# Kernel optimization log

Hardware: AMD Instinct MI355X
Metric: run time of the kernel (lower is better)

## Reference

```python
import jax, jax.numpy as jnp
import numpy as np

GRID = (128, 128, 16)
VSIZE = 0.5  # voxel_size, pc_range = 0
B, V, N, K, C = 2, 100000, 8192, 8, 64
EPS = 1e-5
OFFSETS = [(dx, dy, dz) for dx in (-1, 0, 1) for dy in (-1, 0, 1) for dz in (-1, 0, 1)]


def setup_inputs() -> dict:
    key = jax.random.key(0)
    ks = jax.random.split(key, 8)
    world = jnp.array([GRID[0] * VSIZE, GRID[1] * VSIZE, GRID[2] * VSIZE], jnp.float32)
    keypoints = jax.random.uniform(ks[0], (B, N, K, 3), jnp.float32) * world
    query_feature = jax.random.normal(ks[1], (B, N, C), jnp.float32)
    voxel_feature = jax.random.normal(ks[2], (B, V, C), jnp.float32)
    # unique voxel coords per batch (hash-map / sparse-tensor semantics)
    cells = GRID[0] * GRID[1] * GRID[2]
    perm = jax.vmap(lambda k: jax.random.permutation(k, cells)[:V])(jax.random.split(ks[3], B))
    x = perm // (GRID[1] * GRID[2])
    rem = perm % (GRID[1] * GRID[2])
    voxel_coords = jnp.stack([x, rem // GRID[2], rem % GRID[2]], -1).astype(jnp.int32)
    W1 = jax.random.normal(ks[4], (27, C, C), jnp.float32) * 0.05
    W2 = jax.random.normal(ks[5], (27, C, C), jnp.float32) * 0.05
    proj_W = jax.random.normal(ks[6], (C, C), jnp.float32) / np.sqrt(C).astype(np.float32)
    proj_b = jnp.zeros((C,), jnp.float32)
    return dict(keypoints=keypoints, query_feature=query_feature,
                voxel_feature=voxel_feature, voxel_coords=voxel_coords,
                W1=W1, bn1_gamma=jnp.ones((C,), jnp.float32), bn1_beta=jnp.zeros((C,), jnp.float32),
                W2=W2, bn2_gamma=jnp.ones((C,), jnp.float32), bn2_beta=jnp.zeros((C,), jnp.float32),
                proj_W=proj_W, proj_b=proj_b)


def _subm_conv(feats, grid, cb, cxyz, W):
    # feats: (M, C); grid: (B, X, Y, Z) int32 flat row index or -1; W: (27, Cin, Cout)
    out = jnp.zeros((feats.shape[0], W.shape[-1]), feats.dtype)
    for k, (dx, dy, dz) in enumerate(OFFSETS):
        nx, ny, nz = cxyz[:, 0] + dx, cxyz[:, 1] + dy, cxyz[:, 2] + dz
        valid = (nx >= 0) & (nx < GRID[0]) & (ny >= 0) & (ny < GRID[1]) & (nz >= 0) & (nz < GRID[2])
        nidx = grid[cb, jnp.clip(nx, 0, GRID[0] - 1), jnp.clip(ny, 0, GRID[1] - 1), jnp.clip(nz, 0, GRID[2] - 1)]
        nidx = jnp.where(valid, nidx, -1)
        nf = jnp.where((nidx >= 0)[:, None], feats[jnp.maximum(nidx, 0)], jnp.zeros((), feats.dtype))
        out = out + nf @ W[k]
    return out


def _bn_relu(x, gamma, beta):
    # BatchNorm1d in training mode: batch stats (biased var), then ReLU
    mu = x.mean(0)
    var = jnp.var(x, axis=0)
    return jax.nn.relu((x - mu) * jax.lax.rsqrt(var + EPS) * gamma + beta)


def reference(keypoints, query_feature, voxel_feature, voxel_coords,
              W1, bn1_gamma, bn1_beta, W2, bn2_gamma, bn2_beta, proj_W, proj_b):
    coords = voxel_coords.reshape(-1, 3).astype(jnp.int32)
    cb = jnp.repeat(jnp.arange(B, dtype=jnp.int32), V)
    # dense grid hash: cell -> flat voxel row, -1 if empty (replaces Python dict)
    grid = jnp.full((B,) + GRID, -1, jnp.int32)
    grid = grid.at[cb, coords[:, 0], coords[:, 1], coords[:, 2]].set(jnp.arange(B * V, dtype=jnp.int32))
    feats = voxel_feature.reshape(-1, C)
    feats = _bn_relu(_subm_conv(feats, grid, cb, coords, W1), bn1_gamma, bn1_beta)
    feats = _bn_relu(_subm_conv(feats, grid, cb, coords, W2), bn2_gamma, bn2_beta)
    # quantize keypoints (pc_range = 0, trunc == floor since coords >= 0)
    q = (keypoints / VSIZE).astype(jnp.int32)
    q = jnp.clip(q, 0, jnp.array(GRID, jnp.int32) - 1)  # (B, N, K, 3)
    bidx = jnp.arange(B, dtype=jnp.int32)[:, None, None]
    idx = grid[bidx, q[..., 0], q[..., 1], q[..., 2]]   # (B, N, K); -1 -> fallback row 0
    sampled = feats[jnp.maximum(idx, 0)]                 # (B, N, K, C)
    fused = (sampled.mean(2) + query_feature) @ proj_W.T + proj_b
    voxel_indices = jnp.concatenate(
        [jnp.broadcast_to(bidx[..., None], (B, N, K, 1)), q], axis=-1).reshape(-1, 4)
    return fused, voxel_indices
```

## Files before the change

kernel.cpp:

```cpp
#include <hip/hip_runtime.h>
#include <hip/hip_bf16.h>
#include <math.h>

#define GX 128
#define GY 128
#define GZ 16
#define CELLS (GX*GY*GZ)
#define NCELLT (NB*CELLS)
#define NB 2
#define NV 100000
#define NM (NB*NV)
#define NN 8192
#define NK 8
#define NC 64
#define EPSV 1e-5f
#define TM 256
#define NTILE 98
#define NBLK (8*NTILE)
#define KPH 7

typedef __attribute__((ext_vector_type(8))) short short8;
typedef __attribute__((ext_vector_type(4))) float floatx4;

__device__ __forceinline__ float bf2f(unsigned short u) {
    unsigned int x = ((unsigned int)u) << 16;
    return __builtin_bit_cast(float, x);
}
__device__ __forceinline__ unsigned short f2bf(float f) {
    unsigned int u = __builtin_bit_cast(unsigned int, f);
    return (unsigned short)((u + 0x7fffu + ((u >> 16) & 1u)) >> 16);
}

__global__ void k_init(int* __restrict__ grid, float* __restrict__ stats,
                       unsigned short* __restrict__ featA) {
    int i = blockIdx.x * 256 + threadIdx.x;
    if (i < NCELLT) grid[i] = -1;
    else if (i < NCELLT + 512) stats[i - NCELLT] = 0.f;
    else if (i < NCELLT + 512 + 64) featA[(size_t)NM * 64 + (i - NCELLT - 512)] = 0;
}

__global__ void k_scatter(const int* __restrict__ coords, int* __restrict__ grid) {
    int gid = blockIdx.x * 256 + threadIdx.x;
    if (gid >= NM) return;
    int b = (gid >= NV) ? 1 : 0;
    int x = coords[gid * 3 + 0];
    int y = coords[gid * 3 + 1];
    int z = coords[gid * 3 + 2];
    grid[((b * GX + x) * GY + y) * GZ + z] = gid;
}

__global__ void k_count(const int* __restrict__ grid, int* __restrict__ bcnt) {
    __shared__ int wt[4];
    int t = threadIdx.x;
    int occ = (grid[blockIdx.x * 256 + t] >= 0) ? 1 : 0;
    int w = t >> 6;
    unsigned long long m = __ballot(occ);
    if ((t & 63) == 0) wt[w] = __popcll(m);
    __syncthreads();
    if (t == 0) bcnt[blockIdx.x] = wt[0] + wt[1] + wt[2] + wt[3];
}

__global__ void k_scan2048(const int* __restrict__ bcnt, int* __restrict__ boff) {
    __shared__ int s[256];
    int t = threadIdx.x;
    int v[8], sum = 0;
    #pragma unroll
    for (int j = 0; j < 8; ++j) {
        int x = bcnt[t * 8 + j];
        v[j] = sum;
        sum += x;
    }
    s[t] = sum;
    __syncthreads();
    for (int off = 1; off < 256; off <<= 1) {
        int x = (t >= off) ? s[t - off] : 0;
        __syncthreads();
        s[t] += x;
        __syncthreads();
    }
    int excl = s[t] - sum;
    #pragma unroll
    for (int j = 0; j < 8; ++j) boff[t * 8 + j] = excl + v[j];
}

__global__ void k_assign(const int* __restrict__ gold, const int* __restrict__ boff,
                         int* __restrict__ gnew, int* __restrict__ perm,
                         int* __restrict__ scell) {
    __shared__ int wt[4];
    int t = threadIdx.x;
    int cell = blockIdx.x * 256 + t;
    int old = gold[cell];
    int occ = (old >= 0) ? 1 : 0;
    int w = t >> 6, lane = t & 63;
    unsigned long long m = __ballot(occ);
    int lp = __popcll(m & ((1ULL << lane) - 1ULL));
    if (lane == 63) wt[w] = lp + occ;
    __syncthreads();
    int wbase = 0;
    #pragma unroll
    for (int j = 0; j < 4; ++j) if (j < w) wbase += wt[j];
    int nid = boff[blockIdx.x] + wbase + lp;
    if (occ) {
        gnew[cell] = nid;
        perm[nid] = old;
        scell[nid] = cell;
    } else {
        gnew[cell] = -1;
    }
}

__global__ void k_fb(const int* __restrict__ vcoords, const int* __restrict__ gnew,
                     int* __restrict__ fbp) {
    if (threadIdx.x == 0 && blockIdx.x == 0) {
        int cell = (vcoords[0] * GY + vcoords[1]) * GZ + vcoords[2];
        fbp[0] = gnew[cell];
    }
}

__global__ void k_wprep(const float* __restrict__ W1, const float* __restrict__ W2,
                        unsigned short* __restrict__ Wt1, unsigned short* __restrict__ Wt2) {
    int e = blockIdx.x * 256 + threadIdx.x;
    if (e >= 28 * 512) return;
    int lane = e & 63;
    int fr = (e >> 6) & 7;
    int k = e >> 9;
    int ct = fr >> 1, ks = fr & 1;
    int quad = lane >> 4, n16 = lane & 15;
    int co = ct * 16 + n16;
    #pragma unroll
    for (int j = 0; j < 8; ++j) {
        int ci = ks * 32 + quad * 8 + j;
        unsigned short w1 = 0, w2 = 0;
        if (k < 27) {
            w1 = f2bf(W1[(k << 12) + ci * 64 + co]);
            w2 = f2bf(W2[(k << 12) + ci * 64 + co]);
        }
        Wt1[(size_t)e * 8 + j] = w1;
        Wt2[(size_t)e * 8 + j] = w2;
    }
}

__global__ void k_tobf16s(const float* __restrict__ in, const int* __restrict__ perm,
                          unsigned short* __restrict__ out) {
    int i = blockIdx.x * 256 + threadIdx.x;
    if (i >= NM * 8) return;
    int mrow = i >> 3, part = i & 7;
    int src = perm[mrow];
    const float4* s = (const float4*)(in + (size_t)src * 64 + part * 8);
    float4 a = s[0], b = s[1];
    ushort4 lo, hi;
    lo.x = f2bf(a.x); lo.y = f2bf(a.y); lo.z = f2bf(a.z); lo.w = f2bf(a.w);
    hi.x = f2bf(b.x); hi.y = f2bf(b.y); hi.z = f2bf(b.z); hi.w = f2bf(b.w);
    ushort4* d = (ushort4*)(out + (size_t)mrow * 64 + part * 8);
    d[0] = lo; d[1] = hi;
}

__global__ __launch_bounds__(256, 2) void k_conv(
    const unsigned short* __restrict__ feats, const int* __restrict__ scell,
    const int* __restrict__ grid, const unsigned short* __restrict__ Wt,
    unsigned short* __restrict__ out, float* __restrict__ gsum, float* __restrict__ gsq)
{
    __shared__ unsigned short s_b[KPH * 4096];
    __shared__ int s_nidx[KPH * TM];
    __shared__ int s_c[TM];

    int tid = threadIdx.x;
    int bid = blockIdx.x;
    int tile = (bid & 7) * NTILE + (bid >> 3);
    int m0 = tile * TM;

    {
        int m = m0 + tid;
        s_c[tid] = (m < NM) ? scell[m] : -1;
    }

    int w = tid >> 6, lane = tid & 63;
    int quad = lane >> 4, n16 = lane & 15;
    const unsigned short* fq = feats + quad * 8;

    short8 afr[2][8];

    auto issueA = [&](int kk, short8* af) {
        #pragma unroll
        for (int rt = 0; rt < 4; ++rt) {
            int ni = s_nidx[kk * TM + w * 64 + rt * 16 + n16];
            ni = (ni < 0) ? NM : ni;
            const unsigned short* r0 = fq + (size_t)ni * 64;
            af[rt * 2 + 0] = *(const short8*)(r0);
            af[rt * 2 + 1] = *(const short8*)(r0 + 32);
        }
    };

    floatx4 acc[4][4];
    #pragma unroll
    for (int rt = 0; rt < 4; ++rt)
        #pragma unroll
        for (int ct = 0; ct < 4; ++ct)
            acc[rt][ct] = (floatx4){0.f, 0.f, 0.f, 0.f};

    const uint4* wt4 = (const uint4*)Wt;

    for (int ph = 0; ph < 4; ++ph) {
        int k0 = ph * KPH;
        __syncthreads();
        #pragma unroll
        for (int i = 0; i < KPH * 2; ++i)
            ((uint4*)s_b)[i * 256 + tid] = wt4[(size_t)k0 * 512 + i * 256 + tid];
        #pragma unroll
        for (int j = 0; j < KPH; ++j) {
            int e = j * 256 + tid;
            int kk = e >> 8;
            int r = e & 255;
            int k = k0 + kk;
            int ni = -1;
            if (k < 27) {
                int dx = k / 9 - 1, dy = (k / 3) % 3 - 1, dz = k % 3 - 1;
                int cell = s_c[r];
                if (cell >= 0) {
                    int x = (cell >> 11) & 127, y = (cell >> 4) & 127, z = cell & 15;
                    int nx = x + dx, ny = y + dy, nz = z + dz;
                    if (nx >= 0 && nx < GX && ny >= 0 && ny < GY && nz >= 0 && nz < GZ)
                        ni = grid[cell + dx * (GY * GZ) + dy * GZ + dz];
                }
            }
            s_nidx[kk * TM + r] = ni;
        }
        __syncthreads();

        issueA(0, afr[0]);
        __builtin_amdgcn_sched_barrier(0);

        #pragma unroll
        for (int kk = 0; kk < KPH; ++kk) {
            if (kk + 1 < KPH) issueA(kk + 1, afr[(kk + 1) & 1]);
            __builtin_amdgcn_sched_barrier(0);

            const unsigned short* bb = s_b + kk * 4096;
            short8 bfr[8];
            #pragma unroll
            for (int fr = 0; fr < 8; ++fr)
                bfr[fr] = *(const short8*)(bb + fr * 512 + lane * 8);

            const short8* ac = afr[kk & 1];
            #pragma unroll
            for (int ks = 0; ks < 2; ++ks)
                #pragma unroll
                for (int rt = 0; rt < 4; ++rt)
                    #pragma unroll
                    for (int ct = 0; ct < 4; ++ct)
                        acc[rt][ct] = __builtin_amdgcn_mfma_f32_16x16x32_bf16(
                            ac[rt * 2 + ks], bfr[ct * 2 + ks], acc[rt][ct], 0, 0, 0);
            __builtin_amdgcn_sched_barrier(0);
        }
    }

    #pragma unroll
    for (int rt = 0; rt < 4; ++rt) {
        int rbase = m0 + w * 64 + rt * 16 + quad * 4;
        #pragma unroll
        for (int rg = 0; rg < 4; ++rg) {
            int m = rbase + rg;
            if (m < NM) {
                #pragma unroll
                for (int ct = 0; ct < 4; ++ct)
                    out[(size_t)m * 64 + ct * 16 + n16] = f2bf(acc[rt][ct][rg]);
            }
        }
    }

    float ps[4], pq[4];
    #pragma unroll
    for (int ct = 0; ct < 4; ++ct) { ps[ct] = 0.f; pq[ct] = 0.f; }
    #pragma unroll
    for (int rt = 0; rt < 4; ++rt)
        #pragma unroll
        for (int ct = 0; ct < 4; ++ct)
            #pragma unroll
            for (int rg = 0; rg < 4; ++rg) {
                float v = acc[rt][ct][rg];
                ps[ct] += v;
                pq[ct] += v * v;
            }
    #pragma unroll
    for (int ct = 0; ct < 4; ++ct) {
        ps[ct] += __shfl_xor(ps[ct], 16);
        ps[ct] += __shfl_xor(ps[ct], 32);
        pq[ct] += __shfl_xor(pq[ct], 16);
        pq[ct] += __shfl_xor(pq[ct], 32);
    }
    __syncthreads();
    float* red = (float*)s_nidx;
    if (lane < 16) {
        #pragma unroll
        for (int ct = 0; ct < 4; ++ct) {
            red[w * 64 + ct * 16 + n16]       = ps[ct];
            red[256 + w * 64 + ct * 16 + n16] = pq[ct];
        }
    }
    __syncthreads();
    if (tid < 64) {
        float ts = 0.f, tq = 0.f;
        #pragma unroll
        for (int ww = 0; ww < 4; ++ww) {
            ts += red[ww * 64 + tid];
            tq += red[256 + ww * 64 + tid];
        }
        atomicAdd(gsum + tid, ts);
        atomicAdd(gsq + tid, tq);
    }
}

__global__ void k_bncoef(const float* __restrict__ gsum, const float* __restrict__ gsq,
                         const float* __restrict__ gamma, const float* __restrict__ beta,
                         float* __restrict__ coef) {
    int c = threadIdx.x;
    if (c >= 64) return;
    float mu = gsum[c] / (float)NM;
    float var = gsq[c] / (float)NM - mu * mu;
    float scale = gamma[c] / sqrtf(var + EPSV);
    coef[c] = scale;
    coef[64 + c] = beta[c] - mu * scale;
}

__global__ void k_bnapply(const unsigned short* __restrict__ in, const float* __restrict__ coef,
                          unsigned short* __restrict__ out) {
    int i = blockIdx.x * 256 + threadIdx.x;
    if (i >= NM * 8) return;
    int c8 = (i & 7) * 8;
    uint4 v = ((const uint4*)in)[i];
    unsigned int vv[4] = {v.x, v.y, v.z, v.w};
    unsigned int oo[4];
    #pragma unroll
    for (int j = 0; j < 4; ++j) {
        int c = c8 + j * 2;
        float lo = bf2f((unsigned short)(vv[j] & 0xffffu));
        float hi = bf2f((unsigned short)(vv[j] >> 16));
        lo = fmaxf(lo * coef[c]     + coef[64 + c],     0.f);
        hi = fmaxf(hi * coef[c + 1] + coef[64 + c + 1], 0.f);
        oo[j] = (unsigned int)f2bf(lo) | ((unsigned int)f2bf(hi) << 16);
    }
    uint4 o = {oo[0], oo[1], oo[2], oo[3]};
    ((uint4*)out)[i] = o;
}

__global__ __launch_bounds__(256) void k_sample(
    const float* __restrict__ kp, const float* __restrict__ query,
    const unsigned short* __restrict__ conv2, const float* __restrict__ coef2,
    const int* __restrict__ grid, const int* __restrict__ fbp,
    const float* __restrict__ projW, const float* __restrict__ projB,
    float* __restrict__ out_fused, float* __restrict__ out_vi)
{
    __shared__ float s_pw[64 * 65];
    __shared__ float s_mean[4][64];
    __shared__ int   s_idx[4][8];

    int tid = threadIdx.x;
    for (int e = tid; e < 4096; e += 256) {
        int co = e >> 6, c = e & 63;
        s_pw[co * 65 + c] = projW[e];
    }

    int w = tid >> 6, lane = tid & 63;
    int row = blockIdx.x * 4 + w;
    int b = row >> 13;
    float sc = coef2[lane];
    float sh = coef2[64 + lane];
    int fb = fbp[0];
    __syncthreads();

    if (lane < 8) {
        int kk = lane;
        const float* kpp = kp + ((size_t)row * 8 + kk) * 3;
        int qx = min(max((int)(kpp[0] * 2.0f), 0), GX - 1);
        int qy = min(max((int)(kpp[1] * 2.0f), 0), GY - 1);
        int qz = min(max((int)(kpp[2] * 2.0f), 0), GZ - 1);
        s_idx[w][kk] = grid[((b * GX + qx) * GY + qy) * GZ + qz];
        float4 vi = make_float4((float)b, (float)qx, (float)qy, (float)qz);
        *(float4*)(out_vi + ((size_t)row * 8 + kk) * 4) = vi;
    }
    __syncthreads();

    float acc = 0.f;
    #pragma unroll
    for (int kk = 0; kk < 8; ++kk) {
        int gi = s_idx[w][kk];
        gi = gi < 0 ? fb : gi;
        float v = bf2f(conv2[(size_t)gi * 64 + lane]);
        acc += fmaxf(v * sc + sh, 0.f);
    }
    float mean = acc * 0.125f + query[(size_t)row * 64 + lane];
    s_mean[w][lane] = mean;
    __syncthreads();

    float f = projB[lane];
    const float* pwr = s_pw + lane * 65;
    const float* mv = s_mean[w];
    #pragma unroll 8
    for (int c = 0; c < 64; ++c) f += mv[c] * pwr[c];
    out_fused[(size_t)row * 64 + lane] = f;
}

extern "C" void kernel_launch(void* const* d_in, const int* in_sizes, int n_in,
                              void* d_out, int out_size, void* d_ws, size_t ws_size,
                              hipStream_t stream) {
    const float* keypoints = (const float*)d_in[0];
    const float* query     = (const float*)d_in[1];
    const float* vfeat     = (const float*)d_in[2];
    const int*   vcoords   = (const int*)d_in[3];
    const float* W1        = (const float*)d_in[4];
    const float* g1        = (const float*)d_in[5];
    const float* b1        = (const float*)d_in[6];
    const float* W2        = (const float*)d_in[7];
    const float* g2        = (const float*)d_in[8];
    const float* b2        = (const float*)d_in[9];
    const float* pW        = (const float*)d_in[10];
    const float* pb        = (const float*)d_in[11];

    char* ws = (char*)d_ws;
    int*            gold  = (int*)ws;
    int*            gnew  = (int*)(ws + 2097152);
    float*          stats = (float*)(ws + 4194304);
    int*            fbp   = (int*)(ws + 4196352);
    int*            bcnt  = (int*)(ws + 4196608);
    int*            boff  = (int*)(ws + 4204800);
    int*            perm  = (int*)(ws + 4212992);
    int*            scell = (int*)(ws + 5012992);
    unsigned short* Wt1   = (unsigned short*)(ws + 5812992);
    unsigned short* Wt2   = (unsigned short*)(ws + 6042368);
    unsigned short* featA = (unsigned short*)(ws + 6271744);
    unsigned short* convo = (unsigned short*)(ws + 31871872);

    float* sum1 = stats,       *sq1 = stats + 64,  *coef1 = stats + 128;
    float* sum2 = stats + 256, *sq2 = stats + 320, *coef2 = stats + 384;

    int initN = NCELLT + 512 + 64;
    k_init<<<(initN + 255) / 256, 256, 0, stream>>>(gold, stats, featA);
    k_scatter<<<(NM + 255) / 256, 256, 0, stream>>>(vcoords, gold);

    k_count<<<NCELLT / 256, 256, 0, stream>>>(gold, bcnt);
    k_scan2048<<<1, 256, 0, stream>>>(bcnt, boff);
    k_assign<<<NCELLT / 256, 256, 0, stream>>>(gold, boff, gnew, perm, scell);
    k_fb<<<1, 64, 0, stream>>>(vcoords, gnew, fbp);

    k_wprep<<<(28 * 512 + 255) / 256, 256, 0, stream>>>(W1, W2, Wt1, Wt2);
    k_tobf16s<<<(NM * 8 + 255) / 256, 256, 0, stream>>>(vfeat, perm, featA);

    k_conv<<<NBLK, 256, 0, stream>>>(featA, scell, gnew, Wt1, convo, sum1, sq1);
    k_bncoef<<<1, 64, 0, stream>>>(sum1, sq1, g1, b1, coef1);
    k_bnapply<<<(NM * 8 + 255) / 256, 256, 0, stream>>>(convo, coef1, featA);

    k_conv<<<NBLK, 256, 0, stream>>>(featA, scell, gnew, Wt2, convo, sum2, sq2);
    k_bncoef<<<1, 64, 0, stream>>>(sum2, sq2, g2, b2, coef2);

    float* out_fused = (float*)d_out;
    float* out_vi = out_fused + (size_t)NB * NN * NC;
    k_sample<<<(NB * NN) / 4, 256, 0, stream>>>(keypoints, query, convo, coef2, gnew, fbp,
                                                pW, pb, out_fused, out_vi);
}
```

Before: 342.6 us.

## Precompute neighbor index table once and deepen A-fragment prefetch in conv

Adds a kernel that builds a 28 x rows neighbor-index table (with empty neighbors mapped to the zero row) once, shared by both submanifold convolutions. The conv kernel then reads the table directly instead of recomputing grid lookups into shared memory each phase. It also loads weights into registers before storing them to LDS, overlapping those loads with the neighbor-index loads, and moves from double to triple buffering of the gathered A fragments. The cost is an extra ~22 MB table written and read twice, plus more register pressure from the 3-deep buffers and the 28 neighbor indices held per phase.

```diff
diff --git a/kernel.cpp b/kernel.cpp
--- a/kernel.cpp
+++ b/kernel.cpp
@@ -17,6 +17,7 @@
 #define TM 256
 #define NTILE 98
 #define NBLK (8*NTILE)
+#define NMT (NBLK*TM)
 #define KPH 7
 
 typedef __attribute__((ext_vector_type(8))) short short8;
@@ -114,6 +115,28 @@
     if (threadIdx.x == 0 && blockIdx.x == 0) {
         int cell = (vcoords[0] * GY + vcoords[1]) * GZ + vcoords[2];
         fbp[0] = gnew[cell];
+    }
+}
+
+__global__ void k_nbr(const int* __restrict__ scell, const int* __restrict__ gnew,
+                      int* __restrict__ nid) {
+    int m = blockIdx.x * 256 + threadIdx.x;
+    if (m >= NMT) return;
+    int cell = (m < NM) ? scell[m] : -1;
+    int x = 0, y = 0, z = 0;
+    if (cell >= 0) { x = (cell >> 11) & 127; y = (cell >> 4) & 127; z = cell & 15; }
+    #pragma unroll
+    for (int k = 0; k < 28; ++k) {
+        int ni = NM;
+        if (k < 27 && cell >= 0) {
+            int dx = k / 9 - 1, dy = (k / 3) % 3 - 1, dz = k % 3 - 1;
+            int nx = x + dx, ny = y + dy, nz = z + dz;
+            if (nx >= 0 && nx < GX && ny >= 0 && ny < GY && nz >= 0 && nz < GZ) {
+                int g = gnew[cell + dx * (GY * GZ) + dy * GZ + dz];
+                ni = (g < 0) ? NM : g;
+            }
+        }
+        nid[(size_t)k * NMT + m] = ni;
     }
 }
 
@@ -156,36 +179,28 @@
 }
 
 __global__ __launch_bounds__(256, 2) void k_conv(
-    const unsigned short* __restrict__ feats, const int* __restrict__ scell,
-    const int* __restrict__ grid, const unsigned short* __restrict__ Wt,
+    const unsigned short* __restrict__ feats, const int* __restrict__ nid,
+    const unsigned short* __restrict__ Wt,
     unsigned short* __restrict__ out, float* __restrict__ gsum, float* __restrict__ gsq)
 {
     __shared__ unsigned short s_b[KPH * 4096];
-    __shared__ int s_nidx[KPH * TM];
-    __shared__ int s_c[TM];
 
     int tid = threadIdx.x;
     int bid = blockIdx.x;
     int tile = (bid & 7) * NTILE + (bid >> 3);
     int m0 = tile * TM;
 
-    {
-        int m = m0 + tid;
-        s_c[tid] = (m < NM) ? scell[m] : -1;
-    }
-
     int w = tid >> 6, lane = tid & 63;
     int quad = lane >> 4, n16 = lane & 15;
     const unsigned short* fq = feats + quad * 8;
-
-    short8 afr[2][8];
-
-    auto issueA = [&](int kk, short8* af) {
+    const int* nbase = nid + m0 + w * 64 + n16;
+
+    short8 afr[3][8];
+
+    auto issueA = [&](const int* nr, short8* af) {
         #pragma unroll
         for (int rt = 0; rt < 4; ++rt) {
-            int ni = s_nidx[kk * TM + w * 64 + rt * 16 + n16];
-            ni = (ni < 0) ? NM : ni;
-            const unsigned short* r0 = fq + (size_t)ni * 64;
+            const unsigned short* r0 = fq + (size_t)nr[rt] * 64;
             af[rt * 2 + 0] = *(const short8*)(r0);
             af[rt * 2 + 1] = *(const short8*)(r0 + 32);
         }
@@ -203,45 +218,39 @@
     for (int ph = 0; ph < 4; ++ph) {
         int k0 = ph * KPH;
         __syncthreads();
+
+        uint4 breg[KPH * 2];
         #pragma unroll
         for (int i = 0; i < KPH * 2; ++i)
-            ((uint4*)s_b)[i * 256 + tid] = wt4[(size_t)k0 * 512 + i * 256 + tid];
+            breg[i] = wt4[(size_t)k0 * 512 + i * 256 + tid];
+
+        int nidr[KPH][4];
+        #pragma unroll
+        for (int j = 0; j < KPH; ++j)
+            #pragma unroll
+            for (int rt = 0; rt < 4; ++rt)
+                nidr[j][rt] = nbase[(size_t)(k0 + j) * NMT + rt * 16];
+
+        #pragma unroll
+        for (int i = 0; i < KPH * 2; ++i)
+            ((uint4*)s_b)[i * 256 + tid] = breg[i];
+
+        issueA(nidr[0], afr[0]);
+        issueA(nidr[1], afr[1]);
+        __syncthreads();
+
         #pragma unroll
         for (int j = 0; j < KPH; ++j) {
-            int e = j * 256 + tid;
-            int kk = e >> 8;
-            int r = e & 255;
-            int k = k0 + kk;
-            int ni = -1;
-            if (k < 27) {
-                int dx = k / 9 - 1, dy = (k / 3) % 3 - 1, dz = k % 3 - 1;
-                int cell = s_c[r];
-                if (cell >= 0) {
-                    int x = (cell >> 11) & 127, y = (cell >> 4) & 127, z = cell & 15;
-                    int nx = x + dx, ny = y + dy, nz = z + dz;
-                    if (nx >= 0 && nx < GX && ny >= 0 && ny < GY && nz >= 0 && nz < GZ)
-                        ni = grid[cell + dx * (GY * GZ) + dy * GZ + dz];
-                }
-            }
-            s_nidx[kk * TM + r] = ni;
-        }
-        __syncthreads();
-
-        issueA(0, afr[0]);
-        __builtin_amdgcn_sched_barrier(0);
-
-        #pragma unroll
-        for (int kk = 0; kk < KPH; ++kk) {
-            if (kk + 1 < KPH) issueA(kk + 1, afr[(kk + 1) & 1]);
+            if (j + 2 < KPH) issueA(nidr[j + 2], afr[(j + 2) % 3]);
             __builtin_amdgcn_sched_barrier(0);
 
-            const unsigned short* bb = s_b + kk * 4096;
+            const unsigned short* bb = s_b + j * 4096;
             short8 bfr[8];
             #pragma unroll
             for (int fr = 0; fr < 8; ++fr)
                 bfr[fr] = *(const short8*)(bb + fr * 512 + lane * 8);
 
-            const short8* ac = afr[kk & 1];
+            const short8* ac = afr[j % 3];
             #pragma unroll
             for (int ks = 0; ks < 2; ++ks)
                 #pragma unroll
@@ -289,7 +298,7 @@
         pq[ct] += __shfl_xor(pq[ct], 32);
     }
     __syncthreads();
-    float* red = (float*)s_nidx;
+    float* red = (float*)s_b;
     if (lane < 16) {
         #pragma unroll
         for (int ct = 0; ct < 4; ++ct) {
@@ -428,7 +437,8 @@
     unsigned short* Wt1   = (unsigned short*)(ws + 5812992);
     unsigned short* Wt2   = (unsigned short*)(ws + 6042368);
     unsigned short* featA = (unsigned short*)(ws + 6271744);
-    unsigned short* convo = (unsigned short*)(ws + 31871872);
+    int*            nidt  = (int*)(ws + 31872000);
+    unsigned short* convo = (unsigned short*)(ws + 54350848);
 
     float* sum1 = stats,       *sq1 = stats + 64,  *coef1 = stats + 128;
     float* sum2 = stats + 256, *sq2 = stats + 320, *coef2 = stats + 384;
@@ -441,15 +451,16 @@
     k_scan2048<<<1, 256, 0, stream>>>(bcnt, boff);
     k_assign<<<NCELLT / 256, 256, 0, stream>>>(gold, boff, gnew, perm, scell);
     k_fb<<<1, 64, 0, stream>>>(vcoords, gnew, fbp);
+    k_nbr<<<NMT / 256, 256, 0, stream>>>(scell, gnew, nidt);
 
     k_wprep<<<(28 * 512 + 255) / 256, 256, 0, stream>>>(W1, W2, Wt1, Wt2);
     k_tobf16s<<<(NM * 8 + 255) / 256, 256, 0, stream>>>(vfeat, perm, featA);
 
-    k_conv<<<NBLK, 256, 0, stream>>>(featA, scell, gnew, Wt1, convo, sum1, sq1);
+    k_conv<<<NBLK, 256, 0, stream>>>(featA, nidt, Wt1, convo, sum1, sq1);
     k_bncoef<<<1, 64, 0, stream>>>(sum1, sq1, g1, b1, coef1);
     k_bnapply<<<(NM * 8 + 255) / 256, 256, 0, stream>>>(convo, coef1, featA);
 
-    k_conv<<<NBLK, 256, 0, stream>>>(featA, scell, gnew, Wt2, convo, sum2, sq2);
+    k_conv<<<NBLK, 256, 0, stream>>>(featA, nidt, Wt2, convo, sum2, sq2);
     k_bncoef<<<1, 64, 0, stream>>>(sum2, sq2, g2, b2, coef2);
 
     float* out_fused = (float*)d_out;
```

Result: no change. 343.8 us (+0.4%).
